# Optimization experiments

Measured on AMD Instinct MI355X. Metric: run time of the kernel, lower is better.

Reference implementation:

```python
import jax, jax.numpy as jnp
import numpy as np

EPS = 1e-5


def _bn(h, gamma, beta):
    # training-mode batchnorm over (N, T, V) per channel, NCHW layout
    mean = h.mean(axis=(0, 2, 3), keepdims=True)
    var = h.var(axis=(0, 2, 3), keepdims=True)
    return (h - mean) * jax.lax.rsqrt(var + EPS) * gamma[None, :, None, None] + beta[None, :, None, None]


def setup_inputs() -> dict:
    key = jax.random.key(0)
    ks = jax.random.split(key, 4)
    N, C, T, V, S, K = 64, 64, 300, 25, 3, 9
    x = jax.random.normal(ks[0], (N, C, T, V), jnp.float32)
    A = jax.random.uniform(ks[1], (S, V, V), jnp.float32)
    graph_attn = jnp.ones((S, V, V), jnp.float32)  # init.constant_(1)
    wg = jax.random.normal(ks[2], (S, C, C), jnp.float32) * 0.05  # 1x1 convs per subset [S, Cout, Cin]
    bg = jnp.zeros((S, C), jnp.float32)
    gamma1 = jnp.ones((C,), jnp.float32)
    beta1 = jnp.zeros((C,), jnp.float32)
    wt = jax.random.normal(ks[3], (C, C, K, 1), jnp.float32) * 0.05  # temporal conv [Cout, Cin, K, 1]
    bt = jnp.zeros((C,), jnp.float32)
    gamma2 = jnp.ones((C,), jnp.float32)
    beta2 = jnp.zeros((C,), jnp.float32)
    return dict(x=x, A=A, graph_attn=graph_attn, wg=wg, bg=bg,
                gamma1=gamma1, beta1=beta1, wt=wt, bt=bt,
                gamma2=gamma2, beta2=beta2)


def reference(x, A, graph_attn, wg, bg, gamma1, beta1, wt, bt, gamma2, beta2):
    # ---- GraphConvolution ----
    Ae = A * graph_attn                                   # [S, V, V]
    # per-subset: (x @ A[s]) then 1x1 conv, summed over subsets
    xa = jnp.einsum('nctv,svw->snctw', x, Ae)             # [S, N, C, T, V]
    h = jnp.einsum('snctw,soc->notw', xa, wg)             # [N, Cout, T, V]
    h = h + bg.sum(0)[None, :, None, None]
    h = _bn(h, gamma1, beta1)
    h = jax.nn.relu(h + x)                                # gcn residual (in==out -> identity)
    # ---- CoTemporalConvolution (offline equivalent, kernel (9,1), pad (4,0)) ----
    y = jax.lax.conv_general_dilated(h, wt, window_strides=(1, 1),
                                     padding=((4, 4), (0, 0)))
    y = y + bt[None, :, None, None]
    y = _bn(y, gamma2, beta2)
    # ---- block residual (Delay == identity once streams are aligned) + relu ----
    return jax.nn.relu(y + x)
```

## Files before the change

kernel.cpp:

```cpp
#include <hip/hip_runtime.h>


#define EPSV 1e-5f
#define TVN 7500
#define NTVf 480000.0f
#define TOTE 30720000

#define HPRE_OFF 0
#define AE_OFF   30720000
#define W2T_OFF  30721920
#define WTT_OFF  30734208
#define BSUM_OFF 30771072
#define SCSH_OFF 30771136
#define STAT_OFF 30771392

typedef __attribute__((ext_vector_type(8))) short short8v;
typedef __attribute__((ext_vector_type(4))) float f32x4;

__device__ __forceinline__ unsigned short f2bf(float f) {
  unsigned u = __float_as_uint(f);
  u += 0x7fffu + ((u >> 16) & 1u);
  return (unsigned short)(u >> 16);
}

__global__ __launch_bounds__(256) void k0_prep(
    const float* __restrict__ A, const float* __restrict__ attn,
    const float* __restrict__ wg, const float* __restrict__ bg,
    const float* __restrict__ wt, float* __restrict__ ws) {
  int i = blockIdx.x * 256 + threadIdx.x;
  int stride = gridDim.x * 256;
  for (int j = i; j < 1875; j += stride) ws[AE_OFF + j] = A[j] * attn[j];
  for (int j = i; j < 12288; j += stride) {
    int s = j >> 12, r = j & 4095, c = r >> 6, o = r & 63;
    ws[W2T_OFF + j] = wg[(s << 12) + (o << 6) + c];
  }
  unsigned short* wA16 = (unsigned short*)(ws + WTT_OFF);
  for (int j = i; j < 36864; j += stride) {
    int c = j & 31, o = (j >> 5) & 63, chkt = j >> 11;
    int ch = chkt & 1, kt = chkt >> 1;
    float f = wt[((o << 6) + (ch << 5) + c) * 9 + kt];
    unsigned short hi = f2bf(f);
    float lo = f - __uint_as_float((unsigned)hi << 16);
    wA16[j] = hi;
    wA16[36864 + j] = f2bf(lo);
  }
  for (int j = i; j < 64; j += stride)
    ws[BSUM_OFF + j] = bg[j] + bg[64 + j] + bg[128 + j];
  for (int j = i; j < 256; j += stride) ws[STAT_OFF + j] = 0.f;
}

__global__ __launch_bounds__(512) void k1_gcn(
    const float* __restrict__ x, const float* __restrict__ Ae,
    const float* __restrict__ W2T, const float* __restrict__ bsum,
    float* __restrict__ hpre, float* __restrict__ stat1) {
  const int tb = blockIdx.x;
  const int n = blockIdx.y;
  const int tid = threadIdx.x;
  __shared__ float xs[64 * 101];
  __shared__ float xa[64 * 100];
  __shared__ float ps[64 * 26];
  __shared__ float pq[64 * 26];
  const int colbase = tb * 100;

  for (int ch = tid; ch < 1600; ch += 512) {
    int c = ch / 25, qd = (ch % 25) * 4;
    const float4 v4 = *(const float4*)(x + (n * 64 + c) * TVN + colbase + qd);
    int b = c * 101 + qd;
    xs[b] = v4.x; xs[b + 1] = v4.y; xs[b + 2] = v4.z; xs[b + 3] = v4.w;
  }

  const int og = tid & 15, cg = tid >> 4;
  const int o0 = og * 4, col0 = cg * 4;
  float acc[4][4];
#pragma unroll
  for (int i = 0; i < 4; ++i)
#pragma unroll
    for (int j = 0; j < 4; ++j) acc[i][j] = 0.f;

  for (int s = 0; s < 3; ++s) {
    __syncthreads();
    if (tid < 256) {
      const int c = tid & 63, tt = tid >> 6;
      float aw[25];
#pragma unroll
      for (int w = 0; w < 25; ++w) aw[w] = 0.f;
#pragma unroll
      for (int v = 0; v < 25; ++v) {
        const float xv = xs[c * 101 + tt * 25 + v];
#pragma unroll
        for (int w = 0; w < 25; ++w)
          aw[w] += xv * Ae[(s * 25 + v) * 25 + w];
      }
#pragma unroll
      for (int w = 0; w < 25; ++w) xa[c * 100 + tt * 25 + w] = aw[w];
    }
    __syncthreads();
    if (cg < 25) {
#pragma unroll 4
      for (int c = 0; c < 64; ++c) {
        const float4 a4 = *(const float4*)(W2T + (s * 64 + c) * 64 + o0);
        const float4 b4 = *(const float4*)(&xa[c * 100 + col0]);
        acc[0][0] += a4.x * b4.x; acc[0][1] += a4.x * b4.y; acc[0][2] += a4.x * b4.z; acc[0][3] += a4.x * b4.w;
        acc[1][0] += a4.y * b4.x; acc[1][1] += a4.y * b4.y; acc[1][2] += a4.y * b4.z; acc[1][3] += a4.y * b4.w;
        acc[2][0] += a4.z * b4.x; acc[2][1] += a4.z * b4.y; acc[2][2] += a4.z * b4.z; acc[2][3] += a4.z * b4.w;
        acc[3][0] += a4.w * b4.x; acc[3][1] += a4.w * b4.y; acc[3][2] += a4.w * b4.z; acc[3][3] += a4.w * b4.w;
      }
    }
  }

  if (cg < 25) {
#pragma unroll
    for (int i = 0; i < 4; ++i) {
      const float bo = bsum[o0 + i];
      float4 v;
      v.x = acc[i][0] + bo; v.y = acc[i][1] + bo; v.z = acc[i][2] + bo; v.w = acc[i][3] + bo;
      *(float4*)(hpre + (n * 64 + o0 + i) * TVN + colbase + col0) = v;
      ps[(o0 + i) * 26 + cg] = v.x + v.y + v.z + v.w;
      pq[(o0 + i) * 26 + cg] = v.x * v.x + v.y * v.y + v.z * v.z + v.w * v.w;
    }
  }
  __syncthreads();
  if (tid < 64) {
    float s1 = 0.f, q1 = 0.f;
    for (int g = 0; g < 25; ++g) { s1 += ps[tid * 26 + g]; q1 += pq[tid * 26 + g]; }
    atomicAdd(stat1 + tid, s1);
    atomicAdd(stat1 + 64 + tid, q1);
  }
}

__global__ __launch_bounds__(64) void k2_fin(
    const float* __restrict__ gamma, const float* __restrict__ beta,
    const float* __restrict__ stat, float* __restrict__ scsh) {
  const int o = threadIdx.x;
  double s = (double)stat[o], q = (double)stat[64 + o];
  double mean = s / (double)NTVf;
  double var = q / (double)NTVf - mean * mean;
  float sc = (float)((double)gamma[o] / sqrt(var + (double)EPSV));
  scsh[o] = sc;
  scsh[64 + o] = beta[o] - (float)mean * sc;
}

__global__ __launch_bounds__(256) void k3_conv(
    const float* __restrict__ x, const float* __restrict__ hpre,
    const unsigned short* __restrict__ wAh, const unsigned short* __restrict__ wAl,
    const float* __restrict__ bt, const float* __restrict__ scsh1,
    float* __restrict__ out, float* __restrict__ stat2) {
  const int cb = blockIdx.x;
  const int n = blockIdx.y;
  const int tid = threadIdx.x;
  const int lane = tid & 63, w = tid >> 6;
  const int l15 = lane & 15, q = lane >> 4;
  const int kb8 = q * 8;
  const int outbase = cb * 192;

  __shared__ __align__(16) short smem[2 * 392 * 40];
  short* hh = smem;
  short* hl = smem + 392 * 40;

  f32x4 acc[4][3];
#pragma unroll
  for (int m = 0; m < 4; ++m)
#pragma unroll
    for (int nt = 0; nt < 3; ++nt) {
      f32x4 z = {0.f, 0.f, 0.f, 0.f};
      acc[m][nt] = z;
    }

  for (int ch = 0; ch < 2; ++ch) {
    __syncthreads();
    for (int u = tid; u < 3136; u += 256) {
      const int s = u % 392, cq = u / 392;
      const int gc = outbase - 100 + s;
      const int cbase = ch * 32 + cq * 4;
      short4 vh, vl;
      if (gc >= 0 && gc < TVN) {
#pragma unroll
        for (int i = 0; i < 4; ++i) {
          const int c = cbase + i;
          const float h = hpre[(n * 64 + c) * TVN + gc];
          const float xv = x[(n * 64 + c) * TVN + gc];
          const float r = fmaxf(fmaf(h, scsh1[c], scsh1[64 + c]) + xv, 0.f);
          const unsigned short hi = f2bf(r);
          const float lo = r - __uint_as_float((unsigned)hi << 16);
          ((unsigned short*)&vh)[i] = hi;
          ((unsigned short*)&vl)[i] = f2bf(lo);
        }
      } else {
        vh.x = 0; vh.y = 0; vh.z = 0; vh.w = 0;
        vl.x = 0; vl.y = 0; vl.z = 0; vl.w = 0;
      }
      *(short4*)(hh + s * 40 + cq * 4) = vh;
      *(short4*)(hl + s * 40 + cq * 4) = vl;
    }
    __syncthreads();

#pragma unroll 3
    for (int kt = 0; kt < 9; ++kt) {
      short8v ah[4], al[4], bh[3], bl[3];
      const int abase = (kt * 2 + ch) * 2048;
#pragma unroll
      for (int m = 0; m < 4; ++m) {
        const int aoff = abase + (m * 16 + l15) * 32 + kb8;
        ah[m] = *(const short8v*)(wAh + aoff);
        al[m] = *(const short8v*)(wAl + aoff);
      }
#pragma unroll
      for (int nt = 0; nt < 3; ++nt) {
        const int s = w * 48 + nt * 16 + l15 + kt * 25;
        const int boff = s * 40 + kb8;
        bh[nt] = *(const short8v*)(hh + boff);
        bl[nt] = *(const short8v*)(hl + boff);
      }
#pragma unroll
      for (int m = 0; m < 4; ++m)
#pragma unroll
        for (int nt = 0; nt < 3; ++nt) {
          acc[m][nt] = __builtin_amdgcn_mfma_f32_16x16x32_bf16(ah[m], bh[nt], acc[m][nt], 0, 0, 0);
          acc[m][nt] = __builtin_amdgcn_mfma_f32_16x16x32_bf16(ah[m], bl[nt], acc[m][nt], 0, 0, 0);
          acc[m][nt] = __builtin_amdgcn_mfma_f32_16x16x32_bf16(al[m], bh[nt], acc[m][nt], 0, 0, 0);
        }
    }
  }

  __syncthreads();
  float* ps = (float*)smem;
  float* pq = ps + 64 * 65;
  const int g = w * 16 + l15;
#pragma unroll
  for (int m = 0; m < 4; ++m)
#pragma unroll
    for (int r = 0; r < 4; ++r) {
      const int o = m * 16 + q * 4 + r;
      const float bo = bt[o];
      float ssum = 0.f, ssq = 0.f;
#pragma unroll
      for (int nt = 0; nt < 3; ++nt) {
        const int col = outbase + (w * 3 + nt) * 16 + l15;
        if (col < TVN) {
          const float v = acc[m][nt][r] + bo;
          out[(n * 64 + o) * TVN + col] = v;
          ssum += v; ssq += v * v;
        }
      }
      ps[o * 65 + g] = ssum;
      pq[o * 65 + g] = ssq;
    }
  __syncthreads();
  if (tid < 64) {
    float s2 = 0.f, q2 = 0.f;
    for (int gg = 0; gg < 64; ++gg) { s2 += ps[tid * 65 + gg]; q2 += pq[tid * 65 + gg]; }
    atomicAdd(stat2 + tid, s2);
    atomicAdd(stat2 + 64 + tid, q2);
  }
}

__global__ __launch_bounds__(256) void k5_final(
    const float* __restrict__ x, const float* __restrict__ scsh2,
    float* __restrict__ out) {
  const int total = TOTE / 4;
  for (int ch = blockIdx.x * 256 + threadIdx.x; ch < total; ch += gridDim.x * 256) {
    const int f = ch * 4;
    const int o = (f / TVN) & 63;
    const float sc = scsh2[o], sh = scsh2[64 + o];
    float4 y4 = *(float4*)(out + f);
    const float4 x4 = *(const float4*)(x + f);
    y4.x = fmaxf(fmaf(y4.x, sc, sh) + x4.x, 0.f);
    y4.y = fmaxf(fmaf(y4.y, sc, sh) + x4.y, 0.f);
    y4.z = fmaxf(fmaf(y4.z, sc, sh) + x4.z, 0.f);
    y4.w = fmaxf(fmaf(y4.w, sc, sh) + x4.w, 0.f);
    *(float4*)(out + f) = y4;
  }
}

extern "C" void kernel_launch(void* const* d_in, const int* in_sizes, int n_in,
                              void* d_out, int out_size, void* d_ws, size_t ws_size,
                              hipStream_t stream) {
  const float* x      = (const float*)d_in[0];
  const float* A      = (const float*)d_in[1];
  const float* attn   = (const float*)d_in[2];
  const float* wg     = (const float*)d_in[3];
  const float* bg     = (const float*)d_in[4];
  const float* gamma1 = (const float*)d_in[5];
  const float* beta1  = (const float*)d_in[6];
  const float* wt     = (const float*)d_in[7];
  const float* bt     = (const float*)d_in[8];
  const float* gamma2 = (const float*)d_in[9];
  const float* beta2  = (const float*)d_in[10];
  float* ws = (float*)d_ws;
  float* out = (float*)d_out;
  const unsigned short* wAh = (const unsigned short*)(ws + WTT_OFF);
  const unsigned short* wAl = wAh + 36864;

  k0_prep<<<64, 256, 0, stream>>>(A, attn, wg, bg, wt, ws);
  k1_gcn<<<dim3(75, 64), 512, 0, stream>>>(
      x, ws + AE_OFF, ws + W2T_OFF, ws + BSUM_OFF, ws + HPRE_OFF, ws + STAT_OFF);
  k2_fin<<<1, 64, 0, stream>>>(gamma1, beta1, ws + STAT_OFF, ws + SCSH_OFF);
  k3_conv<<<dim3(40, 64), 256, 0, stream>>>(
      x, ws + HPRE_OFF, wAh, wAl, bt, ws + SCSH_OFF, out, ws + STAT_OFF + 128);
  k2_fin<<<1, 64, 0, stream>>>(gamma2, beta2, ws + STAT_OFF + 128, ws + SCSH_OFF + 128);
  k5_final<<<2048, 256, 0, stream>>>(x, ws + SCSH_OFF + 128, out);
}
```

Measured before the change: 854.7 us.

## Move graph conv to bf16x3 MFMA with prepacked Ae and wg fragments

Rewrites the GCN kernel so both the V×V graph aggregation and the 1x1 channel mixing run on 16x16x32 bf16 MFMA instructions. Each operand is split into hi/lo bf16 parts and three products are summed to keep near-fp32 accuracy. The prep kernel now packs Ae and wg into fragment layouts. Tiles change to 8 timesteps per 256-thread block, and the intermediate goes through LDS as bf16 hi/lo. This replaces scalar FP32 FMA loops, at the cost of triple MFMA work, extra split conversions and uncoalesced scalar x loads and hpre stores.

```diff
diff --git a/kernel.cpp b/kernel.cpp
--- a/kernel.cpp
+++ b/kernel.cpp
@@ -7,12 +7,12 @@
 #define TOTE 30720000
 
 #define HPRE_OFF 0
-#define AE_OFF   30720000
-#define W2T_OFF  30721920
-#define WTT_OFF  30734208
-#define BSUM_OFF 30771072
-#define SCSH_OFF 30771136
-#define STAT_OFF 30771392
+#define WTT_OFF  30720000
+#define AEP_OFF  30756864
+#define WGP_OFF  30759936
+#define BSUM_OFF 30772224
+#define SCSH_OFF 30772288
+#define STAT_OFF 30772544
 
 typedef __attribute__((ext_vector_type(8))) short short8v;
 typedef __attribute__((ext_vector_type(4))) float f32x4;
@@ -21,6 +21,9 @@
   unsigned u = __float_as_uint(f);
   u += 0x7fffu + ((u >> 16) & 1u);
   return (unsigned short)(u >> 16);
+}
+__device__ __forceinline__ float bf2f(unsigned short h) {
+  return __uint_as_float((unsigned)h << 16);
 }
 
 __global__ __launch_bounds__(256) void k0_prep(
@@ -29,102 +32,187 @@
     const float* __restrict__ wt, float* __restrict__ ws) {
   int i = blockIdx.x * 256 + threadIdx.x;
   int stride = gridDim.x * 256;
-  for (int j = i; j < 1875; j += stride) ws[AE_OFF + j] = A[j] * attn[j];
-  for (int j = i; j < 12288; j += stride) {
-    int s = j >> 12, r = j & 4095, c = r >> 6, o = r & 63;
-    ws[W2T_OFF + j] = wg[(s << 12) + (o << 6) + c];
-  }
   unsigned short* wA16 = (unsigned short*)(ws + WTT_OFF);
   for (int j = i; j < 36864; j += stride) {
     int c = j & 31, o = (j >> 5) & 63, chkt = j >> 11;
     int ch = chkt & 1, kt = chkt >> 1;
     float f = wt[((o << 6) + (ch << 5) + c) * 9 + kt];
     unsigned short hi = f2bf(f);
-    float lo = f - __uint_as_float((unsigned)hi << 16);
     wA16[j] = hi;
-    wA16[36864 + j] = f2bf(lo);
+    wA16[36864 + j] = f2bf(f - bf2f(hi));
+  }
+  unsigned short* AePh = (unsigned short*)(ws + AEP_OFF);
+  unsigned short* AePl = AePh + 3072;
+  for (int j = i; j < 3072; j += stride) {
+    int e = j & 7, l = (j >> 3) & 63, nb = (j >> 9) & 1, s = j >> 10;
+    int v = (l >> 4) * 8 + e, wv = nb * 16 + (l & 15);
+    float val = (v < 25 && wv < 25) ? A[(s * 25 + v) * 25 + wv] * attn[(s * 25 + v) * 25 + wv] : 0.f;
+    unsigned short hi = f2bf(val);
+    AePh[j] = hi;
+    AePl[j] = f2bf(val - bf2f(hi));
+  }
+  unsigned short* WgPh = (unsigned short*)(ws + WGP_OFF);
+  unsigned short* WgPl = WgPh + 12288;
+  for (int j = i; j < 12288; j += stride) {
+    int e = j & 7, l = (j >> 3) & 63, ks = (j >> 9) & 1, mt = (j >> 10) & 3, s = j >> 12;
+    int o = mt * 16 + (l & 15), c = ks * 32 + (l >> 4) * 8 + e;
+    float val = wg[(s * 64 + o) * 64 + c];
+    unsigned short hi = f2bf(val);
+    WgPh[j] = hi;
+    WgPl[j] = f2bf(val - bf2f(hi));
   }
   for (int j = i; j < 64; j += stride)
     ws[BSUM_OFF + j] = bg[j] + bg[64 + j] + bg[128 + j];
   for (int j = i; j < 256; j += stride) ws[STAT_OFF + j] = 0.f;
 }
 
-__global__ __launch_bounds__(512) void k1_gcn(
-    const float* __restrict__ x, const float* __restrict__ Ae,
-    const float* __restrict__ W2T, const float* __restrict__ bsum,
-    float* __restrict__ hpre, float* __restrict__ stat1) {
+__global__ __launch_bounds__(256) void k1_gcn(
+    const float* __restrict__ x,
+    const unsigned short* __restrict__ AePh, const unsigned short* __restrict__ AePl,
+    const unsigned short* __restrict__ WgPh, const unsigned short* __restrict__ WgPl,
+    const float* __restrict__ bsum, float* __restrict__ hpre,
+    float* __restrict__ stat1) {
   const int tb = blockIdx.x;
   const int n = blockIdx.y;
   const int tid = threadIdx.x;
-  __shared__ float xs[64 * 101];
-  __shared__ float xa[64 * 100];
-  __shared__ float ps[64 * 26];
-  __shared__ float pq[64 * 26];
-  const int colbase = tb * 100;
-
-  for (int ch = tid; ch < 1600; ch += 512) {
-    int c = ch / 25, qd = (ch % 25) * 4;
-    const float4 v4 = *(const float4*)(x + (n * 64 + c) * TVN + colbase + qd);
-    int b = c * 101 + qd;
-    xs[b] = v4.x; xs[b + 1] = v4.y; xs[b + 2] = v4.z; xs[b + 3] = v4.w;
-  }
-
-  const int og = tid & 15, cg = tid >> 4;
-  const int o0 = og * 4, col0 = cg * 4;
-  float acc[4][4];
-#pragma unroll
-  for (int i = 0; i < 4; ++i)
-#pragma unroll
-    for (int j = 0; j < 4; ++j) acc[i][j] = 0.f;
+  const int lane = tid & 63, w = tid >> 6;
+  const int l15 = lane & 15, q = lane >> 4;
+  const int wm = w & 1, wn = w >> 1;
+  const int t0 = tb * 8;
+
+  __shared__ __align__(16) short Bhi[208 * 72];
+  __shared__ __align__(16) short Blo[208 * 72];
+  __shared__ float ps[128], pq[128];
+
+  short8v xh[8], xl[8];
+#pragma unroll
+  for (int i = 0; i < 8; ++i) {
+    const int id = w * 8 + i;
+    const int tl = id >> 2, cc = id & 3;
+    const int c = cc * 16 + l15;
+    const int t = t0 + tl;
+    const float* base = x + (n * 64 + c) * TVN + t * 25;
+    const bool tok = (t < 300);
+#pragma unroll
+    for (int e = 0; e < 8; ++e) {
+      const int v = q * 8 + e;
+      const float xv = (tok && v < 25) ? base[v] : 0.f;
+      const unsigned short hi = f2bf(xv);
+      ((unsigned short*)&xh[i])[e] = hi;
+      ((unsigned short*)&xl[i])[e] = f2bf(xv - bf2f(hi));
+    }
+  }
+
+  f32x4 acc[2][7];
+#pragma unroll
+  for (int i = 0; i < 2; ++i)
+#pragma unroll
+    for (int j = 0; j < 7; ++j) {
+      f32x4 z = {0.f, 0.f, 0.f, 0.f};
+      acc[i][j] = z;
+    }
 
   for (int s = 0; s < 3; ++s) {
     __syncthreads();
-    if (tid < 256) {
-      const int c = tid & 63, tt = tid >> 6;
-      float aw[25];
-#pragma unroll
-      for (int w = 0; w < 25; ++w) aw[w] = 0.f;
-#pragma unroll
-      for (int v = 0; v < 25; ++v) {
-        const float xv = xs[c * 101 + tt * 25 + v];
-#pragma unroll
-        for (int w = 0; w < 25; ++w)
-          aw[w] += xv * Ae[(s * 25 + v) * 25 + w];
-      }
-#pragma unroll
-      for (int w = 0; w < 25; ++w) xa[c * 100 + tt * 25 + w] = aw[w];
+    short8v aeh[2], ael[2];
+#pragma unroll
+    for (int nb = 0; nb < 2; ++nb) {
+      const int off = ((s * 2 + nb) * 64 + lane) * 8;
+      aeh[nb] = *(const short8v*)(AePh + off);
+      ael[nb] = *(const short8v*)(AePl + off);
+    }
+#pragma unroll
+    for (int i = 0; i < 8; ++i) {
+      const int id = w * 8 + i;
+      const int tl = id >> 2, cc = id & 3;
+      f32x4 d[2];
+#pragma unroll
+      for (int nb = 0; nb < 2; ++nb) {
+        f32x4 z = {0.f, 0.f, 0.f, 0.f};
+        z = __builtin_amdgcn_mfma_f32_16x16x32_bf16(xh[i], aeh[nb], z, 0, 0, 0);
+        z = __builtin_amdgcn_mfma_f32_16x16x32_bf16(xh[i], ael[nb], z, 0, 0, 0);
+        z = __builtin_amdgcn_mfma_f32_16x16x32_bf16(xl[i], aeh[nb], z, 0, 0, 0);
+        d[nb] = z;
+      }
+#pragma unroll
+      for (int nb = 0; nb < 2; ++nb) {
+        const int wv = nb * 16 + l15;
+        if (wv < 25) {
+          const int col2 = tl * 25 + wv;
+          const int kbase = cc * 16 + q * 4;
+          short4 h4, l4;
+#pragma unroll
+          for (int r = 0; r < 4; ++r) {
+            const unsigned short hi = f2bf(d[nb][r]);
+            ((unsigned short*)&h4)[r] = hi;
+            ((unsigned short*)&l4)[r] = f2bf(d[nb][r] - bf2f(hi));
+          }
+          *(short4*)(Bhi + col2 * 72 + kbase) = h4;
+          *(short4*)(Blo + col2 * 72 + kbase) = l4;
+        }
+      }
     }
     __syncthreads();
-    if (cg < 25) {
-#pragma unroll 4
-      for (int c = 0; c < 64; ++c) {
-        const float4 a4 = *(const float4*)(W2T + (s * 64 + c) * 64 + o0);
-        const float4 b4 = *(const float4*)(&xa[c * 100 + col0]);
-        acc[0][0] += a4.x * b4.x; acc[0][1] += a4.x * b4.y; acc[0][2] += a4.x * b4.z; acc[0][3] += a4.x * b4.w;
-        acc[1][0] += a4.y * b4.x; acc[1][1] += a4.y * b4.y; acc[1][2] += a4.y * b4.z; acc[1][3] += a4.y * b4.w;
-        acc[2][0] += a4.z * b4.x; acc[2][1] += a4.z * b4.y; acc[2][2] += a4.z * b4.z; acc[2][3] += a4.z * b4.w;
-        acc[3][0] += a4.w * b4.x; acc[3][1] += a4.w * b4.y; acc[3][2] += a4.w * b4.z; acc[3][3] += a4.w * b4.w;
-      }
-    }
-  }
-
-  if (cg < 25) {
-#pragma unroll
-    for (int i = 0; i < 4; ++i) {
-      const float bo = bsum[o0 + i];
-      float4 v;
-      v.x = acc[i][0] + bo; v.y = acc[i][1] + bo; v.z = acc[i][2] + bo; v.w = acc[i][3] + bo;
-      *(float4*)(hpre + (n * 64 + o0 + i) * TVN + colbase + col0) = v;
-      ps[(o0 + i) * 26 + cg] = v.x + v.y + v.z + v.w;
-      pq[(o0 + i) * 26 + cg] = v.x * v.x + v.y * v.y + v.z * v.z + v.w * v.w;
+    short8v wgh[2][2], wgl[2][2];
+#pragma unroll
+    for (int i = 0; i < 2; ++i) {
+      const int mt = wm * 2 + i;
+#pragma unroll
+      for (int ks = 0; ks < 2; ++ks) {
+        const int off = (((s * 4 + mt) * 2 + ks) * 64 + lane) * 8;
+        wgh[i][ks] = *(const short8v*)(WgPh + off);
+        wgl[i][ks] = *(const short8v*)(WgPl + off);
+      }
+    }
+#pragma unroll
+    for (int j = 0; j < 7; ++j) {
+      const int tile = wn * 7 + j;
+      if (tile < 13) {
+#pragma unroll
+        for (int ks = 0; ks < 2; ++ks) {
+          const int boff = (tile * 16 + l15) * 72 + ks * 32 + q * 8;
+          const short8v bh = *(const short8v*)(Bhi + boff);
+          const short8v bl = *(const short8v*)(Blo + boff);
+#pragma unroll
+          for (int i = 0; i < 2; ++i) {
+            acc[i][j] = __builtin_amdgcn_mfma_f32_16x16x32_bf16(wgh[i][ks], bh, acc[i][j], 0, 0, 0);
+            acc[i][j] = __builtin_amdgcn_mfma_f32_16x16x32_bf16(wgh[i][ks], bl, acc[i][j], 0, 0, 0);
+            acc[i][j] = __builtin_amdgcn_mfma_f32_16x16x32_bf16(wgl[i][ks], bh, acc[i][j], 0, 0, 0);
+          }
+        }
+      }
+    }
+  }
+
+#pragma unroll
+  for (int i = 0; i < 2; ++i) {
+    const int mt = wm * 2 + i;
+#pragma unroll
+    for (int r = 0; r < 4; ++r) {
+      const int o = mt * 16 + q * 4 + r;
+      const float bo = bsum[o];
+      float sums = 0.f, sqs = 0.f;
+#pragma unroll
+      for (int j = 0; j < 7; ++j) {
+        const int tile = wn * 7 + j;
+        const int col = tile * 16 + l15;
+        if (tile < 13 && col < 200 && t0 * 25 + col < TVN) {
+          const float v = acc[i][j][r] + bo;
+          hpre[(n * 64 + o) * TVN + t0 * 25 + col] = v;
+          sums += v; sqs += v * v;
+        }
+      }
+      sums += __shfl_xor(sums, 1); sqs += __shfl_xor(sqs, 1);
+      sums += __shfl_xor(sums, 2); sqs += __shfl_xor(sqs, 2);
+      sums += __shfl_xor(sums, 4); sqs += __shfl_xor(sqs, 4);
+      sums += __shfl_xor(sums, 8); sqs += __shfl_xor(sqs, 8);
+      if (l15 == 0) { ps[o * 2 + wn] = sums; pq[o * 2 + wn] = sqs; }
     }
   }
   __syncthreads();
   if (tid < 64) {
-    float s1 = 0.f, q1 = 0.f;
-    for (int g = 0; g < 25; ++g) { s1 += ps[tid * 26 + g]; q1 += pq[tid * 26 + g]; }
-    atomicAdd(stat1 + tid, s1);
-    atomicAdd(stat1 + 64 + tid, q1);
+    atomicAdd(stat1 + tid, ps[tid * 2] + ps[tid * 2 + 1]);
+    atomicAdd(stat1 + 64 + tid, pq[tid * 2] + pq[tid * 2 + 1]);
   }
 }
 
@@ -181,9 +269,8 @@
           const float xv = x[(n * 64 + c) * TVN + gc];
           const float r = fmaxf(fmaf(h, scsh1[c], scsh1[64 + c]) + xv, 0.f);
           const unsigned short hi = f2bf(r);
-          const float lo = r - __uint_as_float((unsigned)hi << 16);
           ((unsigned short*)&vh)[i] = hi;
-          ((unsigned short*)&vl)[i] = f2bf(lo);
+          ((unsigned short*)&vl)[i] = f2bf(r - bf2f(hi));
         }
       } else {
         vh.x = 0; vh.y = 0; vh.z = 0; vh.w = 0;
@@ -288,12 +375,16 @@
   const float* beta2  = (const float*)d_in[10];
   float* ws = (float*)d_ws;
   float* out = (float*)d_out;
-  const unsigned short* wAh = (const unsigned short*)(ws + WTT_OFF);
-  const unsigned short* wAl = wAh + 36864;
+  const unsigned short* wAh  = (const unsigned short*)(ws + WTT_OFF);
+  const unsigned short* wAl  = wAh + 36864;
+  const unsigned short* AePh = (const unsigned short*)(ws + AEP_OFF);
+  const unsigned short* AePl = AePh + 3072;
+  const unsigned short* WgPh = (const unsigned short*)(ws + WGP_OFF);
+  const unsigned short* WgPl = WgPh + 12288;
 
   k0_prep<<<64, 256, 0, stream>>>(A, attn, wg, bg, wt, ws);
-  k1_gcn<<<dim3(75, 64), 512, 0, stream>>>(
-      x, ws + AE_OFF, ws + W2T_OFF, ws + BSUM_OFF, ws + HPRE_OFF, ws + STAT_OFF);
+  k1_gcn<<<dim3(38, 64), 256, 0, stream>>>(
+      x, AePh, AePl, WgPh, WgPl, ws + BSUM_OFF, ws + HPRE_OFF, ws + STAT_OFF);
   k2_fin<<<1, 64, 0, stream>>>(gamma1, beta1, ws + STAT_OFF, ws + SCSH_OFF);
   k3_conv<<<dim3(40, 64), 256, 0, stream>>>(
       x, ws + HPRE_OFF, wAh, wAl, bt, ws + SCSH_OFF, out, ws + STAT_OFF + 128);
```

New measurement: 688.1 us. 19.5% less time.
